# Kernel optimization log

Hardware: AMD Instinct MI355X
Metric: run time of the kernel (lower is better)

## Reference

```python
import jax, jax.numpy as jnp
import numpy as np

B, N, D, H = 4, 4096, 512, 8
K = D // H  # per-head dim = 64


def setup_inputs() -> dict:
    key = jax.random.key(0)
    k1, k2, k3, k4 = jax.random.split(key, 4)
    x = jax.random.normal(k1, (B, N, D), dtype=jnp.float32)
    # Conv1d(D, K, 1, bias=False) -> weight matrix [K, D], kaiming fan_out
    Wa = jax.random.normal(k2, (K, D), dtype=jnp.float32) * np.float32(np.sqrt(2.0 / K))
    # Conv1d(K, 1, 1) -> weight vector [K], bias scalar (init 0.01)
    Wb = jax.random.normal(k3, (K,), dtype=jnp.float32) * np.float32(np.sqrt(2.0))
    Wc = jax.random.normal(k4, (K,), dtype=jnp.float32) * np.float32(np.sqrt(2.0))
    wb_bias = jnp.full((), 0.01, dtype=jnp.float32)
    wc_bias = jnp.full((), 0.01, dtype=jnp.float32)
    bias = jnp.full((K,), 0.01, dtype=jnp.float32)
    return {"batchinput": x, "Wa": Wa, "Wb": Wb, "wb_bias": wb_bias,
            "Wc": Wc, "wc_bias": wc_bias, "bias": bias}


def reference(batchinput, Wa, Wb, wb_bias, Wc, wc_bias, bias):
    # single step (n_steps=1); all n_head heads share weights, so mean over
    # identical heads equals one head (dropout=0.0 -> identity).
    h = jnp.einsum('bnd,kd->bnk', batchinput, Wa)            # [B,N,K] projected feats
    t1 = jnp.einsum('bnk,k->bn', h, Wb) + wb_bias            # [B,N]
    t2 = jnp.einsum('bnk,k->bn', h, Wc) + wc_bias            # [B,N]
    scores = t1[:, :, None] + t2[:, None, :]                 # [B,N,N] additive score
    coefs = jax.nn.softmax(jax.nn.leaky_relu(scores, negative_slope=0.2), axis=-1)
    out = jnp.einsum('bnm,bmk->bnk', coefs, h) + bias        # [B,N,K]
    return out
```

## Files before the change

### kernel.cpp

```cpp
#include <hip/hip_runtime.h>
#include <hip/hip_bf16.h>

constexpr int cB = 4;
constexpr int cN = 4096;
constexpr int cD = 512;
constexpr int cK = 64;
constexpr int cNB = cB * cN;
constexpr int cNP = cN + 1;
constexpr int cCS = 32;
constexpr int cNC = cN / cCS;
constexpr int cNC1 = cNC + 1;

typedef unsigned short u16;
typedef unsigned int u32;
typedef unsigned long long u64;
typedef __bf16 bf16x8 __attribute__((ext_vector_type(8)));
typedef float f32x4 __attribute__((ext_vector_type(4)));

constexpr size_t OFF_H    = 0;
constexpr size_t OFF_T1   = OFF_H    + (size_t)cNB * cK;
constexpr size_t OFF_T2   = OFF_T1   + cNB;
constexpr size_t OFF_T2S  = OFF_T2   + cNB;
constexpr size_t OFF_IDX  = OFF_T2S  + cNB;
constexpr size_t OFF_EPL  = OFF_IDX  + cNB;
constexpr size_t OFF_GNL  = OFF_EPL  + (size_t)cB * cNP * cK;
constexpr size_t OFF_EPS  = OFF_GNL  + (size_t)cB * cNP * cK;
constexpr size_t OFF_GNS  = OFF_EPS  + (size_t)cB * cNP;
constexpr size_t OFF_CHE  = OFF_GNS  + (size_t)cB * cNP;
constexpr size_t OFF_CHG  = OFF_CHE  + (size_t)cB * cNC * cK;
constexpr size_t OFF_CHES = OFF_CHG  + (size_t)cB * cNC * cK;
constexpr size_t OFF_CHGS = OFF_CHES + (size_t)cB * cNC;
constexpr size_t OFF_OFE  = OFF_CHGS + (size_t)cB * cNC;
constexpr size_t OFF_OFG  = OFF_OFE  + (size_t)cB * cNC1 * cK;
constexpr size_t OFF_OFES = OFF_OFG  + (size_t)cB * cNC1 * cK;
constexpr size_t OFF_OFGS = OFF_OFES + (size_t)cB * cNC1;
constexpr size_t OFF_XB16 = OFF_OFGS + (size_t)cB * cNC1;
constexpr size_t OFF_WB16 = OFF_XB16 + (size_t)cNB * cD / 2;

__device__ __forceinline__ u16 f2bf(float f) {
    unsigned u = __float_as_uint(f);
    u += 0x7fffu + ((u >> 16) & 1u);
    return (u16)(u >> 16);
}
__device__ __forceinline__ u32 pk2(float a, float b) {
    return (u32)f2bf(a) | ((u32)f2bf(b) << 16);
}
__device__ __forceinline__ u32 f2sort(float f) {
    u32 b = __float_as_uint(f);
    u32 mask = (u32)((int)b >> 31);
    return b ^ (mask | 0x80000000u);
}

__global__ __launch_bounds__(256) void k_wprep(
    const float* __restrict__ Wa, u16* __restrict__ wab16)
{
    int i4 = (blockIdx.x * 256 + threadIdx.x) * 4;
    float4 v = *(const float4*)(Wa + i4);
    uint2 p = {pk2(v.x, v.y), pk2(v.z, v.w)};
    *(uint2*)(wab16 + i4) = p;
}

__global__ __launch_bounds__(256) void k_prep(
    const float* __restrict__ x, const float* __restrict__ Wa,
    const float* __restrict__ Wb, const float* __restrict__ wbb,
    const float* __restrict__ Wc, const float* __restrict__ wcb,
    u16* __restrict__ xb16, float* __restrict__ t1, float* __restrict__ t2)
{
    __shared__ float wabL[cD], wacL[cD];
    int t = threadIdx.x;
    float s1a = 0.f, s2a = 0.f, s1b = 0.f, s2b = 0.f;
#pragma unroll 8
    for (int k = 0; k < cK; ++k) {
        float wbk = Wb[k], wck = Wc[k];
        float wa1 = Wa[k * cD + t];
        float wa2 = Wa[k * cD + t + 256];
        s1a += wa1 * wbk; s2a += wa1 * wck;
        s1b += wa2 * wbk; s2b += wa2 * wck;
    }
    wabL[t] = s1a; wacL[t] = s2a; wabL[t + 256] = s1b; wacL[t + 256] = s2b;
    __syncthreads();

    int w = t >> 6, lane = t & 63;
    int d1 = lane * 4, d2 = 256 + lane * 4;
    float4 wbA = *(const float4*)&wabL[d1], wbB = *(const float4*)&wabL[d2];
    float4 wcA = *(const float4*)&wacL[d1], wcB = *(const float4*)&wacL[d2];
    float wbbv = wbb[0], wcbv = wcb[0];
#pragma unroll 2
    for (int rr = 0; rr < 8; ++rr) {
        int row = blockIdx.x * 32 + w * 8 + rr;
        const float* xp = x + (size_t)row * cD;
        float4 a  = *(const float4*)(xp + d1);
        float4 bq = *(const float4*)(xp + d2);
        uint2 pa = {pk2(a.x, a.y), pk2(a.z, a.w)};
        uint2 pb = {pk2(bq.x, bq.y), pk2(bq.z, bq.w)};
        *(uint2*)(xb16 + (size_t)row * cD + d1) = pa;
        *(uint2*)(xb16 + (size_t)row * cD + d2) = pb;
        float p1 = a.x*wbA.x + a.y*wbA.y + a.z*wbA.z + a.w*wbA.w
                 + bq.x*wbB.x + bq.y*wbB.y + bq.z*wbB.z + bq.w*wbB.w;
        float p2 = a.x*wcA.x + a.y*wcA.y + a.z*wcA.z + a.w*wcA.w
                 + bq.x*wcB.x + bq.y*wcB.y + bq.z*wcB.z + bq.w*wcB.w;
#pragma unroll
        for (int off = 32; off > 0; off >>= 1) {
            p1 += __shfl_down(p1, off, 64);
            p2 += __shfl_down(p2, off, 64);
        }
        if (lane == 0) { t1[row] = p1 + wbbv; t2[row] = p2 + wcbv; }
    }
}

__global__ __launch_bounds__(256) void k_proj(
    const u16* __restrict__ xb16, const u16* __restrict__ wab16,
    float* __restrict__ h)
{
    __shared__ u16 xs[64 * 32];
    __shared__ u16 was[64 * 32];
    int t = threadIdx.x;
    int rowbase = blockIdx.x * 64;
    int w = t >> 6, lane = t & 63, m = lane & 15, quad = lane >> 4;
    int grow = w * 16 + (lane >> 2);
    int gcol = (lane & 3) * 8;
    const u16* xg = xb16 + (size_t)(rowbase + grow) * cD + gcol;
    const u16* wg = wab16 + (size_t)grow * cD + gcol;
    int lidx = grow * 32 + gcol;

    f32x4 acc[4] = {{0.f,0.f,0.f,0.f},{0.f,0.f,0.f,0.f},
                    {0.f,0.f,0.f,0.f},{0.f,0.f,0.f,0.f}};
    uint4 xv = *(const uint4*)(xg);
    uint4 wv = *(const uint4*)(wg);
    for (int s = 0; s < 16; ++s) {
        __syncthreads();
        *(uint4*)&xs[lidx] = xv;
        *(uint4*)&was[lidx] = wv;
        if (s < 15) {
            xv = *(const uint4*)(xg + (s + 1) * 32);
            wv = *(const uint4*)(wg + (s + 1) * 32);
        }
        __syncthreads();
        bf16x8 av = *(const bf16x8*)&xs[(w * 16 + m) * 32 + quad * 8];
#pragma unroll
        for (int g = 0; g < 4; ++g) {
            bf16x8 bv = *(const bf16x8*)&was[(g * 16 + m) * 32 + quad * 8];
            acc[g] = __builtin_amdgcn_mfma_f32_16x16x32_bf16(av, bv, acc[g], 0, 0, 0);
        }
    }
#pragma unroll
    for (int g = 0; g < 4; ++g) {
#pragma unroll
        for (int r4 = 0; r4 < 4; ++r4) {
            int row = w * 16 + quad * 4 + r4;
            h[(size_t)(rowbase + row) * cK + g * 16 + m] = acc[g][r4];
        }
    }
}

__global__ __launch_bounds__(256) void k_rank(
    const float* __restrict__ t2, float* __restrict__ t2s, int* __restrict__ idxs)
{
    __shared__ u64 keys[cN];
    __shared__ int part[4][64];
    int t = threadIdx.x;
    int b = blockIdx.x >> 6;
    int rowgrp = blockIdx.x & 63;
    for (int i = t; i < cN; i += 256)
        keys[i] = ((u64)f2sort(t2[b * cN + i]) << 32) | (u32)i;
    __syncthreads();
    int lane = t & 63, subset = t >> 6;
    u64 mykey = keys[rowgrp * 64 + lane];
    int s0 = subset * 1024;
    int cnt = 0;
#pragma unroll 8
    for (int kk = 0; kk < 1024; ++kk)
        cnt += (keys[s0 + kk] < mykey) ? 1 : 0;
    part[subset][lane] = cnt;
    __syncthreads();
    if (t < 64) {
        int jj = rowgrp * 64 + t;
        int rank = part[0][t] + part[1][t] + part[2][t] + part[3][t];
        t2s[b * cN + rank] = t2[b * cN + jj];
        idxs[b * cN + rank] = jj;
    }
}

__global__ __launch_bounds__(64) void k_chunkscan(
    const float* __restrict__ t2s, const int* __restrict__ idxs,
    const float* __restrict__ h,
    float* __restrict__ EpL, float* __restrict__ GnL,
    float* __restrict__ eps_l, float* __restrict__ gns_l,
    float* __restrict__ chE, float* __restrict__ chG,
    float* __restrict__ chEs, float* __restrict__ chGs)
{
    int lane = threadIdx.x;
    int blk = blockIdx.x;
    int c = blk & (cNC - 1);
    int type = (blk >> 7) & 1;
    int b = blk >> 8;
    int base = b * cN + c * cCS;
    size_t rowbase = ((size_t)b * cNP + c * cCS) * cK;
    int sbase = b * cNP + c * cCS;
    float M2 = t2s[b * cN + cN - 1];
    int   idxv = (lane < cCS) ? idxs[base + lane] : 0;
    float t2v  = (lane < cCS) ? t2s[base + lane] : 0.f;
    float acc = 0.f, accs = 0.f;

    if (type == 0) {
        if (c == cNC - 1) {
            EpL[((size_t)b * cNP + cN) * cK + lane] = 0.f;
            if (lane == 0) eps_l[b * cNP + cN] = 0.f;
        }
        for (int g = 3; g >= 0; --g) {
            float hv[8];
#pragma unroll
            for (int i = 0; i < 8; ++i) {
                int j = __shfl(idxv, g * 8 + i, 64);
                hv[i] = h[((size_t)b * cN + j) * cK + lane];
            }
#pragma unroll
            for (int i = 7; i >= 0; --i) {
                int q = g * 8 + i;
                float e = __expf(__shfl(t2v, q, 64) - M2);
                acc += e * hv[i]; accs += e;
                EpL[rowbase + (size_t)q * cK + lane] = acc;
                if (lane == 0) eps_l[sbase + q] = accs;
            }
        }
        chE[((size_t)b * cNC + c) * cK + lane] = acc;
        if (lane == 0) chEs[b * cNC + c] = accs;
    } else {
        if (c == cNC - 1) {
            GnL[((size_t)b * cNP + cN) * cK + lane] = 0.f;
            if (lane == 0) gns_l[b * cNP + cN] = 0.f;
        }
        for (int g = 0; g < 4; ++g) {
            float hv[8];
#pragma unroll
            for (int i = 0; i < 8; ++i) {
                int j = __shfl(idxv, g * 8 + i, 64);
                hv[i] = h[((size_t)b * cN + j) * cK + lane];
            }
#pragma unroll
            for (int i = 0; i < 8; ++i) {
                int q = g * 8 + i;
                float gg = __expf(0.2f * (__shfl(t2v, q, 64) - M2));
                GnL[rowbase + (size_t)q * cK + lane] = acc;
                if (lane == 0) gns_l[sbase + q] = accs;
                acc += gg * hv[i]; accs += gg;
            }
        }
        chG[((size_t)b * cNC + c) * cK + lane] = acc;
        if (lane == 0) chGs[b * cNC + c] = accs;
    }
}

__global__ __launch_bounds__(64) void k_offsets(
    const float* __restrict__ chE, const float* __restrict__ chG,
    const float* __restrict__ chEs, const float* __restrict__ chGs,
    float* __restrict__ ofE, float* __restrict__ ofG,
    float* __restrict__ ofEs, float* __restrict__ ofGs)
{
    int lane = threadIdx.x;
    int b = blockIdx.x;
    float acc = 0.f;
    ofE[((size_t)b * cNC1 + cNC) * cK + lane] = 0.f;
    for (int c = cNC - 1; c >= 0; --c) {
        ofE[((size_t)b * cNC1 + c) * cK + lane] = acc;
        acc += chE[((size_t)b * cNC + c) * cK + lane];
    }
    acc = 0.f;
    for (int c = 0; c < cNC; ++c) {
        ofG[((size_t)b * cNC1 + c) * cK + lane] = acc;
        acc += chG[((size_t)b * cNC + c) * cK + lane];
    }
    ofG[((size_t)b * cNC1 + cNC) * cK + lane] = acc;

    float e0 = chEs[b * cNC + 2 * lane], e1 = chEs[b * cNC + 2 * lane + 1];
    float g0 = chGs[b * cNC + 2 * lane], g1 = chGs[b * cNC + 2 * lane + 1];
    float pe = e0 + e1, pg = g0 + g1;
    float se = pe, sg = pg;
#pragma unroll
    for (int off = 1; off < 64; off <<= 1) {
        float te = __shfl_down(se, off, 64);
        if (lane + off < 64) se += te;
        float tg = __shfl_up(sg, off, 64);
        if (lane >= off) sg += tg;
    }
    ofGs[b * cNC1 + 2 * lane]     = sg - pg;
    ofGs[b * cNC1 + 2 * lane + 1] = sg - pg + g0;
    ofEs[b * cNC1 + 2 * lane]     = se - pe + e1;
    ofEs[b * cNC1 + 2 * lane + 1] = se - pe;
    if (lane == 0)  ofEs[b * cNC1 + cNC] = 0.f;
    if (lane == 63) ofGs[b * cNC1 + cNC] = sg;
}

__global__ __launch_bounds__(256) void k_out(
    const float* __restrict__ t1, const float* __restrict__ t2s,
    const float* __restrict__ EpL, const float* __restrict__ GnL,
    const float* __restrict__ eps_l, const float* __restrict__ gns_l,
    const float* __restrict__ ofE, const float* __restrict__ ofG,
    const float* __restrict__ ofEs, const float* __restrict__ ofGs,
    const float* __restrict__ bias, float* __restrict__ out)
{
    int tid = threadIdx.x;
    int lane = tid & 63;
    int r = blockIdx.x * 4 + (tid >> 6);
    int b = r >> 12;
    float T1 = t1[r];
    float M2 = t2s[b * cN + cN - 1];
    float smax = T1 + M2;
    float m = fmaxf(smax, 0.2f * smax);
    float A  = __expf(smax - m);
    float Cc = __expf(0.2f * smax - m);
    float keyv = -T1;
    int lo = 0, hi = cN;
    while (lo < hi) {
        int mid = (lo + hi) >> 1;
        if (t2s[b * cN + mid] < keyv) lo = mid + 1; else hi = mid;
    }
    int p = lo;
    int c = p >> 5;
    size_t pr = ((size_t)b * cNP + p) * cK + lane;
    size_t cr = ((size_t)b * cNC1 + c) * cK + lane;
    float num = A * (EpL[pr] + ofE[cr]) + Cc * (GnL[pr] + ofG[cr]);
    float den = A * (eps_l[(size_t)b * cNP + p] + ofEs[b * cNC1 + c])
              + Cc * (gns_l[(size_t)b * cNP + p] + ofGs[b * cNC1 + c]);
    out[(size_t)r * cK + lane] = num / den + bias[lane];
}

extern "C" void kernel_launch(void* const* d_in, const int* in_sizes, int n_in,
                              void* d_out, int out_size, void* d_ws, size_t ws_size,
                              hipStream_t stream)
{
    const float* x    = (const float*)d_in[0];
    const float* Wa   = (const float*)d_in[1];
    const float* Wb   = (const float*)d_in[2];
    const float* wbb  = (const float*)d_in[3];
    const float* Wc   = (const float*)d_in[4];
    const float* wcb  = (const float*)d_in[5];
    const float* bias = (const float*)d_in[6];
    float* out = (float*)d_out;

    float* ws = (float*)d_ws;
    float* h     = ws + OFF_H;
    float* t1    = ws + OFF_T1;
    float* t2    = ws + OFF_T2;
    float* t2s   = ws + OFF_T2S;
    int*   idxs  = (int*)(ws + OFF_IDX);
    float* EpL   = ws + OFF_EPL;
    float* GnL   = ws + OFF_GNL;
    float* eps_l = ws + OFF_EPS;
    float* gns_l = ws + OFF_GNS;
    float* chE   = ws + OFF_CHE;
    float* chG   = ws + OFF_CHG;
    float* chEs  = ws + OFF_CHES;
    float* chGs  = ws + OFF_CHGS;
    float* ofE   = ws + OFF_OFE;
    float* ofG   = ws + OFF_OFG;
    float* ofEs  = ws + OFF_OFES;
    float* ofGs  = ws + OFF_OFGS;
    u16*   xb16  = (u16*)(ws + OFF_XB16);
    u16*   wab16 = (u16*)(ws + OFF_WB16);

    k_wprep<<<32, 256, 0, stream>>>(Wa, wab16);
    k_prep<<<512, 256, 0, stream>>>(x, Wa, Wb, wbb, Wc, wcb, xb16, t1, t2);
    k_proj<<<256, 256, 0, stream>>>(xb16, wab16, h);
    k_rank<<<256, 256, 0, stream>>>(t2, t2s, idxs);
    k_chunkscan<<<cB * 2 * cNC, 64, 0, stream>>>(t2s, idxs, h, EpL, GnL, eps_l, gns_l,
                                                 chE, chG, chEs, chGs);
    k_offsets<<<cB, 64, 0, stream>>>(chE, chG, chEs, chGs, ofE, ofG, ofEs, ofGs);
    k_out<<<cNB / 4, 256, 0, stream>>>(t1, t2s, EpL, GnL, eps_l, gns_l,
                                       ofE, ofG, ofEs, ofGs, bias, out);
}
```

Baseline: 148.3 us.

## Merge kernel launches, halve scan chunk size, parallelize chunk-offset scan

```diff
diff --git a/kernel.cpp b/kernel.cpp
--- a/kernel.cpp
+++ b/kernel.cpp
@@ -7,7 +7,7 @@
 constexpr int cK = 64;
 constexpr int cNB = cB * cN;
 constexpr int cNP = cN + 1;
-constexpr int cCS = 32;
+constexpr int cCS = 16;
 constexpr int cNC = cN / cCS;
 constexpr int cNC1 = cNC + 1;
 
@@ -51,23 +51,22 @@
     return b ^ (mask | 0x80000000u);
 }
 
-__global__ __launch_bounds__(256) void k_wprep(
-    const float* __restrict__ Wa, u16* __restrict__ wab16)
-{
-    int i4 = (blockIdx.x * 256 + threadIdx.x) * 4;
-    float4 v = *(const float4*)(Wa + i4);
-    uint2 p = {pk2(v.x, v.y), pk2(v.z, v.w)};
-    *(uint2*)(wab16 + i4) = p;
-}
-
 __global__ __launch_bounds__(256) void k_prep(
     const float* __restrict__ x, const float* __restrict__ Wa,
     const float* __restrict__ Wb, const float* __restrict__ wbb,
     const float* __restrict__ Wc, const float* __restrict__ wcb,
-    u16* __restrict__ xb16, float* __restrict__ t1, float* __restrict__ t2)
+    u16* __restrict__ xb16, u16* __restrict__ wab16,
+    float* __restrict__ t1, float* __restrict__ t2)
 {
     __shared__ float wabL[cD], wacL[cD];
     int t = threadIdx.x;
+    if (blockIdx.x >= 512) {
+        int i4 = (((int)blockIdx.x - 512) * 256 + t) * 4;
+        float4 v = *(const float4*)(Wa + i4);
+        uint2 p = {pk2(v.x, v.y), pk2(v.z, v.w)};
+        *(uint2*)(wab16 + i4) = p;
+        return;
+    }
     float s1a = 0.f, s2a = 0.f, s1b = 0.f, s2b = 0.f;
 #pragma unroll 8
     for (int k = 0; k < cK; ++k) {
@@ -108,76 +107,76 @@
     }
 }
 
-__global__ __launch_bounds__(256) void k_proj(
+__global__ __launch_bounds__(256) void k_projrank(
     const u16* __restrict__ xb16, const u16* __restrict__ wab16,
-    float* __restrict__ h)
-{
-    __shared__ u16 xs[64 * 32];
-    __shared__ u16 was[64 * 32];
+    const float* __restrict__ t2,
+    float* __restrict__ h, float* __restrict__ t2s, int* __restrict__ idxs)
+{
+    __shared__ u64 shbuf[4096 + 128];
     int t = threadIdx.x;
-    int rowbase = blockIdx.x * 64;
-    int w = t >> 6, lane = t & 63, m = lane & 15, quad = lane >> 4;
-    int grow = w * 16 + (lane >> 2);
-    int gcol = (lane & 3) * 8;
-    const u16* xg = xb16 + (size_t)(rowbase + grow) * cD + gcol;
-    const u16* wg = wab16 + (size_t)grow * cD + gcol;
-    int lidx = grow * 32 + gcol;
-
-    f32x4 acc[4] = {{0.f,0.f,0.f,0.f},{0.f,0.f,0.f,0.f},
-                    {0.f,0.f,0.f,0.f},{0.f,0.f,0.f,0.f}};
-    uint4 xv = *(const uint4*)(xg);
-    uint4 wv = *(const uint4*)(wg);
-    for (int s = 0; s < 16; ++s) {
+    if (blockIdx.x < 256) {
+        u16* xs = (u16*)shbuf;
+        u16* was = xs + 64 * 32;
+        int rowbase = blockIdx.x * 64;
+        int w = t >> 6, lane = t & 63, m = lane & 15, quad = lane >> 4;
+        int grow = w * 16 + (lane >> 2);
+        int gcol = (lane & 3) * 8;
+        const u16* xg = xb16 + (size_t)(rowbase + grow) * cD + gcol;
+        const u16* wg = wab16 + (size_t)grow * cD + gcol;
+        int lidx = grow * 32 + gcol;
+
+        f32x4 acc[4] = {{0.f,0.f,0.f,0.f},{0.f,0.f,0.f,0.f},
+                        {0.f,0.f,0.f,0.f},{0.f,0.f,0.f,0.f}};
+        uint4 xv = *(const uint4*)(xg);
+        uint4 wv = *(const uint4*)(wg);
+        for (int s = 0; s < 16; ++s) {
+            __syncthreads();
+            *(uint4*)&xs[lidx] = xv;
+            *(uint4*)&was[lidx] = wv;
+            if (s < 15) {
+                xv = *(const uint4*)(xg + (s + 1) * 32);
+                wv = *(const uint4*)(wg + (s + 1) * 32);
+            }
+            __syncthreads();
+            bf16x8 av = *(const bf16x8*)&xs[(w * 16 + m) * 32 + quad * 8];
+#pragma unroll
+            for (int g = 0; g < 4; ++g) {
+                bf16x8 bv = *(const bf16x8*)&was[(g * 16 + m) * 32 + quad * 8];
+                acc[g] = __builtin_amdgcn_mfma_f32_16x16x32_bf16(av, bv, acc[g], 0, 0, 0);
+            }
+        }
+#pragma unroll
+        for (int g = 0; g < 4; ++g) {
+#pragma unroll
+            for (int r4 = 0; r4 < 4; ++r4) {
+                int row = w * 16 + quad * 4 + r4;
+                h[(size_t)(rowbase + row) * cK + g * 16 + m] = acc[g][r4];
+            }
+        }
+    } else {
+        u64* keys = shbuf;
+        int* part = (int*)(shbuf + 4096);
+        int rb = blockIdx.x - 256;
+        int b = rb >> 6;
+        int rowgrp = rb & 63;
+        for (int i = t; i < cN; i += 256)
+            keys[i] = ((u64)f2sort(t2[b * cN + i]) << 32) | (u32)i;
         __syncthreads();
-        *(uint4*)&xs[lidx] = xv;
-        *(uint4*)&was[lidx] = wv;
-        if (s < 15) {
-            xv = *(const uint4*)(xg + (s + 1) * 32);
-            wv = *(const uint4*)(wg + (s + 1) * 32);
-        }
+        int lane = t & 63, subset = t >> 6;
+        u64 mykey = keys[rowgrp * 64 + lane];
+        int s0 = subset * 1024;
+        int cnt = 0;
+#pragma unroll 8
+        for (int kk = 0; kk < 1024; ++kk)
+            cnt += (keys[s0 + kk] < mykey) ? 1 : 0;
+        part[subset * 64 + lane] = cnt;
         __syncthreads();
-        bf16x8 av = *(const bf16x8*)&xs[(w * 16 + m) * 32 + quad * 8];
-#pragma unroll
-        for (int g = 0; g < 4; ++g) {
-            bf16x8 bv = *(const bf16x8*)&was[(g * 16 + m) * 32 + quad * 8];
-            acc[g] = __builtin_amdgcn_mfma_f32_16x16x32_bf16(av, bv, acc[g], 0, 0, 0);
-        }
-    }
-#pragma unroll
-    for (int g = 0; g < 4; ++g) {
-#pragma unroll
-        for (int r4 = 0; r4 < 4; ++r4) {
-            int row = w * 16 + quad * 4 + r4;
-            h[(size_t)(rowbase + row) * cK + g * 16 + m] = acc[g][r4];
-        }
-    }
-}
-
-__global__ __launch_bounds__(256) void k_rank(
-    const float* __restrict__ t2, float* __restrict__ t2s, int* __restrict__ idxs)
-{
-    __shared__ u64 keys[cN];
-    __shared__ int part[4][64];
-    int t = threadIdx.x;
-    int b = blockIdx.x >> 6;
-    int rowgrp = blockIdx.x & 63;
-    for (int i = t; i < cN; i += 256)
-        keys[i] = ((u64)f2sort(t2[b * cN + i]) << 32) | (u32)i;
-    __syncthreads();
-    int lane = t & 63, subset = t >> 6;
-    u64 mykey = keys[rowgrp * 64 + lane];
-    int s0 = subset * 1024;
-    int cnt = 0;
-#pragma unroll 8
-    for (int kk = 0; kk < 1024; ++kk)
-        cnt += (keys[s0 + kk] < mykey) ? 1 : 0;
-    part[subset][lane] = cnt;
-    __syncthreads();
-    if (t < 64) {
-        int jj = rowgrp * 64 + t;
-        int rank = part[0][t] + part[1][t] + part[2][t] + part[3][t];
-        t2s[b * cN + rank] = t2[b * cN + jj];
-        idxs[b * cN + rank] = jj;
+        if (t < 64) {
+            int jj = rowgrp * 64 + t;
+            int rank = part[t] + part[64 + t] + part[128 + t] + part[192 + t];
+            t2s[b * cN + rank] = t2[b * cN + jj];
+            idxs[b * cN + rank] = jj;
+        }
     }
 }
 
@@ -192,7 +191,6 @@
     int lane = threadIdx.x;
     int blk = blockIdx.x;
     int c = blk & (cNC - 1);
-    int type = (blk >> 7) & 1;
     int b = blk >> 8;
     int base = b * cN + c * cCS;
     size_t rowbase = ((size_t)b * cNP + c * cCS) * cK;
@@ -200,95 +198,127 @@
     float M2 = t2s[b * cN + cN - 1];
     int   idxv = (lane < cCS) ? idxs[base + lane] : 0;
     float t2v  = (lane < cCS) ? t2s[base + lane] : 0.f;
+
+    float hv[cCS];
+#pragma unroll
+    for (int i = 0; i < cCS; ++i) {
+        int j = __shfl(idxv, i, 64);
+        hv[i] = h[((size_t)b * cN + j) * cK + lane];
+    }
+    float ee[cCS], gg[cCS];
+#pragma unroll
+    for (int i = 0; i < cCS; ++i) {
+        float d = __shfl(t2v, i, 64) - M2;
+        ee[i] = __expf(d);
+        gg[i] = __expf(0.2f * d);
+    }
+    if (c == cNC - 1) {
+        EpL[((size_t)b * cNP + cN) * cK + lane] = 0.f;
+        GnL[((size_t)b * cNP + cN) * cK + lane] = 0.f;
+        if (lane == 0) { eps_l[b * cNP + cN] = 0.f; gns_l[b * cNP + cN] = 0.f; }
+    }
     float acc = 0.f, accs = 0.f;
-
-    if (type == 0) {
-        if (c == cNC - 1) {
-            EpL[((size_t)b * cNP + cN) * cK + lane] = 0.f;
-            if (lane == 0) eps_l[b * cNP + cN] = 0.f;
-        }
-        for (int g = 3; g >= 0; --g) {
-            float hv[8];
-#pragma unroll
-            for (int i = 0; i < 8; ++i) {
-                int j = __shfl(idxv, g * 8 + i, 64);
-                hv[i] = h[((size_t)b * cN + j) * cK + lane];
-            }
-#pragma unroll
-            for (int i = 7; i >= 0; --i) {
-                int q = g * 8 + i;
-                float e = __expf(__shfl(t2v, q, 64) - M2);
-                acc += e * hv[i]; accs += e;
-                EpL[rowbase + (size_t)q * cK + lane] = acc;
-                if (lane == 0) eps_l[sbase + q] = accs;
-            }
-        }
-        chE[((size_t)b * cNC + c) * cK + lane] = acc;
-        if (lane == 0) chEs[b * cNC + c] = accs;
-    } else {
-        if (c == cNC - 1) {
-            GnL[((size_t)b * cNP + cN) * cK + lane] = 0.f;
-            if (lane == 0) gns_l[b * cNP + cN] = 0.f;
-        }
-        for (int g = 0; g < 4; ++g) {
-            float hv[8];
-#pragma unroll
-            for (int i = 0; i < 8; ++i) {
-                int j = __shfl(idxv, g * 8 + i, 64);
-                hv[i] = h[((size_t)b * cN + j) * cK + lane];
-            }
-#pragma unroll
-            for (int i = 0; i < 8; ++i) {
-                int q = g * 8 + i;
-                float gg = __expf(0.2f * (__shfl(t2v, q, 64) - M2));
-                GnL[rowbase + (size_t)q * cK + lane] = acc;
-                if (lane == 0) gns_l[sbase + q] = accs;
-                acc += gg * hv[i]; accs += gg;
-            }
-        }
-        chG[((size_t)b * cNC + c) * cK + lane] = acc;
-        if (lane == 0) chGs[b * cNC + c] = accs;
-    }
-}
-
-__global__ __launch_bounds__(64) void k_offsets(
+#pragma unroll
+    for (int i = cCS - 1; i >= 0; --i) {
+        acc += ee[i] * hv[i]; accs += ee[i];
+        EpL[rowbase + (size_t)i * cK + lane] = acc;
+        if (lane == 0) eps_l[sbase + i] = accs;
+    }
+    chE[((size_t)b * cNC + c) * cK + lane] = acc;
+    if (lane == 0) chEs[b * cNC + c] = accs;
+    acc = 0.f; accs = 0.f;
+#pragma unroll
+    for (int i = 0; i < cCS; ++i) {
+        GnL[rowbase + (size_t)i * cK + lane] = acc;
+        if (lane == 0) gns_l[sbase + i] = accs;
+        acc += gg[i] * hv[i]; accs += gg[i];
+    }
+    chG[((size_t)b * cNC + c) * cK + lane] = acc;
+    if (lane == 0) chGs[b * cNC + c] = accs;
+}
+
+__global__ __launch_bounds__(256) void k_offsets(
     const float* __restrict__ chE, const float* __restrict__ chG,
     const float* __restrict__ chEs, const float* __restrict__ chGs,
     float* __restrict__ ofE, float* __restrict__ ofG,
     float* __restrict__ ofEs, float* __restrict__ ofGs)
 {
-    int lane = threadIdx.x;
-    int b = blockIdx.x;
-    float acc = 0.f;
-    ofE[((size_t)b * cNC1 + cNC) * cK + lane] = 0.f;
-    for (int c = cNC - 1; c >= 0; --c) {
-        ofE[((size_t)b * cNC1 + c) * cK + lane] = acc;
-        acc += chE[((size_t)b * cNC + c) * cK + lane];
-    }
-    acc = 0.f;
-    for (int c = 0; c < cNC; ++c) {
-        ofG[((size_t)b * cNC1 + c) * cK + lane] = acc;
-        acc += chG[((size_t)b * cNC + c) * cK + lane];
-    }
-    ofG[((size_t)b * cNC1 + cNC) * cK + lane] = acc;
-
-    float e0 = chEs[b * cNC + 2 * lane], e1 = chEs[b * cNC + 2 * lane + 1];
-    float g0 = chGs[b * cNC + 2 * lane], g1 = chGs[b * cNC + 2 * lane + 1];
-    float pe = e0 + e1, pg = g0 + g1;
-    float se = pe, sg = pg;
-#pragma unroll
-    for (int off = 1; off < 64; off <<= 1) {
-        float te = __shfl_down(se, off, 64);
-        if (lane + off < 64) se += te;
-        float tg = __shfl_up(sg, off, 64);
-        if (lane >= off) sg += tg;
-    }
-    ofGs[b * cNC1 + 2 * lane]     = sg - pg;
-    ofGs[b * cNC1 + 2 * lane + 1] = sg - pg + g0;
-    ofEs[b * cNC1 + 2 * lane]     = se - pe + e1;
-    ofEs[b * cNC1 + 2 * lane + 1] = se - pe;
-    if (lane == 0)  ofEs[b * cNC1 + cNC] = 0.f;
-    if (lane == 63) ofGs[b * cNC1 + cNC] = sg;
+    __shared__ float wsum[4][64];
+    int t = threadIdx.x;
+    int lane = t & 63, w = t >> 6;
+    int dir = blockIdx.x & 1;
+    int b = blockIdx.x >> 1;
+    const float* ch = dir ? chG : chE;
+    float* of = dir ? ofG : ofE;
+    int c0 = w * 64;
+
+    float cv[64];
+    float s = 0.f;
+#pragma unroll
+    for (int i = 0; i < 64; ++i) {
+        cv[i] = ch[((size_t)b * cNC + c0 + i) * cK + lane];
+        s += cv[i];
+    }
+    wsum[w][lane] = s;
+    __syncthreads();
+    float base = 0.f;
+    if (dir == 0) { for (int w2 = w + 1; w2 < 4; ++w2) base += wsum[w2][lane]; }
+    else          { for (int w2 = 0; w2 < w; ++w2) base += wsum[w2][lane]; }
+
+    if (dir == 0) {
+        float run = base;
+#pragma unroll
+        for (int i = 63; i >= 0; --i) {
+            of[((size_t)b * cNC1 + c0 + i) * cK + lane] = run;
+            run += cv[i];
+        }
+        if (w == 0) of[((size_t)b * cNC1 + cNC) * cK + lane] = 0.f;
+    } else {
+        float run = base;
+#pragma unroll
+        for (int i = 0; i < 64; ++i) {
+            of[((size_t)b * cNC1 + c0 + i) * cK + lane] = run;
+            run += cv[i];
+        }
+        if (w == 3) of[((size_t)b * cNC1 + cNC) * cK + lane] = run;
+    }
+
+    if (w == 0) {
+        const float* chs = dir ? chGs : chEs;
+        float* ofs = dir ? ofGs : ofEs;
+        float e0 = chs[b * cNC + lane * 4 + 0];
+        float e1 = chs[b * cNC + lane * 4 + 1];
+        float e2 = chs[b * cNC + lane * 4 + 2];
+        float e3 = chs[b * cNC + lane * 4 + 3];
+        float p = e0 + e1 + e2 + e3;
+        if (dir == 0) {
+            float s2 = p;
+#pragma unroll
+            for (int off = 1; off < 64; off <<= 1) {
+                float tv = __shfl_down(s2, off, 64);
+                if (lane + off < 64) s2 += tv;
+            }
+            float excl = s2 - p;
+            ofs[b * cNC1 + lane * 4 + 0] = excl + e1 + e2 + e3;
+            ofs[b * cNC1 + lane * 4 + 1] = excl + e2 + e3;
+            ofs[b * cNC1 + lane * 4 + 2] = excl + e3;
+            ofs[b * cNC1 + lane * 4 + 3] = excl;
+            if (lane == 0) ofs[b * cNC1 + cNC] = 0.f;
+        } else {
+            float s2 = p;
+#pragma unroll
+            for (int off = 1; off < 64; off <<= 1) {
+                float tv = __shfl_up(s2, off, 64);
+                if (lane >= off) s2 += tv;
+            }
+            float excl = s2 - p;
+            ofs[b * cNC1 + lane * 4 + 0] = excl;
+            ofs[b * cNC1 + lane * 4 + 1] = excl + e0;
+            ofs[b * cNC1 + lane * 4 + 2] = excl + e0 + e1;
+            ofs[b * cNC1 + lane * 4 + 3] = excl + e0 + e1 + e2;
+            if (lane == 63) ofs[b * cNC1 + cNC] = s2;
+        }
+    }
 }
 
 __global__ __launch_bounds__(256) void k_out(
@@ -316,7 +346,7 @@
         if (t2s[b * cN + mid] < keyv) lo = mid + 1; else hi = mid;
     }
     int p = lo;
-    int c = p >> 5;
+    int c = p >> 4;
     size_t pr = ((size_t)b * cNP + p) * cK + lane;
     size_t cr = ((size_t)b * cNC1 + c) * cK + lane;
     float num = A * (EpL[pr] + ofE[cr]) + Cc * (GnL[pr] + ofG[cr]);
@@ -359,13 +389,11 @@
     u16*   xb16  = (u16*)(ws + OFF_XB16);
     u16*   wab16 = (u16*)(ws + OFF_WB16);
 
-    k_wprep<<<32, 256, 0, stream>>>(Wa, wab16);
-    k_prep<<<512, 256, 0, stream>>>(x, Wa, Wb, wbb, Wc, wcb, xb16, t1, t2);
-    k_proj<<<256, 256, 0, stream>>>(xb16, wab16, h);
-    k_rank<<<256, 256, 0, stream>>>(t2, t2s, idxs);
-    k_chunkscan<<<cB * 2 * cNC, 64, 0, stream>>>(t2s, idxs, h, EpL, GnL, eps_l, gns_l,
-                                                 chE, chG, chEs, chGs);
-    k_offsets<<<cB, 64, 0, stream>>>(chE, chG, chEs, chGs, ofE, ofG, ofEs, ofGs);
+    k_prep<<<544, 256, 0, stream>>>(x, Wa, Wb, wbb, Wc, wcb, xb16, wab16, t1, t2);
+    k_projrank<<<512, 256, 0, stream>>>(xb16, wab16, t2, h, t2s, idxs);
+    k_chunkscan<<<cB * cNC, 64, 0, stream>>>(t2s, idxs, h, EpL, GnL, eps_l, gns_l,
+                                             chE, chG, chEs, chGs);
+    k_offsets<<<cB * 2, 256, 0, stream>>>(chE, chG, chEs, chGs, ofE, ofG, ofEs, ofGs);
     k_out<<<cNB / 4, 256, 0, stream>>>(t1, t2s, EpL, GnL, eps_l, gns_l,
                                        ofE, ofG, ofEs, ofGs, bias, out);
 }
```

Measured after the change: 132.8 us. 10.4% less time.
